# Kernel tuning notes

Measured on AMD Instinct MI355X. Metric: run time of the kernel, lower is better.

## Reference

```python
import jax, jax.numpy as jnp
import numpy as np

B = 2048      # number of binary mixtures
NPM = 30      # atoms per molecule
N = B * NPM   # total nodes per side
EPM = 120     # directed edges per molecule
IN_DIM = 74
H = 128
NC = 2


def setup_inputs() -> dict:
    key = jax.random.key(0)
    ks = jax.random.split(key, 24)
    rng = np.random.default_rng(0)
    off = np.repeat(np.arange(B, dtype=np.int64) * NPM, EPM)
    mk_idx = lambda: jnp.asarray((rng.integers(0, NPM, B * EPM) + off).astype(np.int32))

    def lin(k, fi, fo):
        return (jax.random.normal(k, (fi, fo), jnp.float32) / np.sqrt(fi)).astype(jnp.float32)

    inp = {
        'h1': jax.random.normal(ks[0], (N, IN_DIM), jnp.float32),
        'h2': jax.random.normal(ks[1], (N, IN_DIM), jnp.float32),
        'solv1_x': jax.random.uniform(ks[2], (B,), jnp.float32),
        'inter_hb': jax.random.uniform(ks[3], (B,), jnp.float32),
        'intra_hb1': jax.random.uniform(ks[4], (B,), jnp.float32),
        'intra_hb2': jax.random.uniform(ks[5], (B,), jnp.float32),
        'Wg1': lin(ks[6], IN_DIM, H), 'bg1': jnp.zeros((H,), jnp.float32),
        'Wg2': lin(ks[7], H, H), 'bg2': jnp.zeros((H,), jnp.float32),
        'Wp': lin(ks[8], H, H), 'bp': jnp.zeros((H,), jnp.float32),
        'We1': lin(ks[9], 1, 32), 'be1': jnp.zeros((32,), jnp.float32),
        'We2': lin(ks[10], 32, H * H), 'be2': jnp.zeros((H * H,), jnp.float32),
        'bnn': jnp.zeros((H,), jnp.float32),
        'Wih': lin(ks[11], H, 3 * H), 'bih': jnp.zeros((3 * H,), jnp.float32),
        'Whh': lin(ks[12], H, 3 * H), 'bhh': jnp.zeros((3 * H,), jnp.float32),
        'Wcl1': lin(ks[13], 2 * H, H), 'bcl1': jnp.zeros((H,), jnp.float32),
        'Wcl2': lin(ks[14], H, H), 'bcl2': jnp.zeros((H,), jnp.float32),
        'Wcl3': lin(ks[15], H, NC), 'bcl3': jnp.zeros((NC,), jnp.float32),
        'src1': mk_idx(), 'dst1': mk_idx(), 'src2': mk_idx(), 'dst2': mk_idx(),
    }
    return inp


def _graphconv(x, src, dst, W, b, n):
    # DGL GraphConv, norm='both': D_in^{-1/2} A D_out^{-1/2} X W + b
    ones = jnp.ones(src.shape[0], x.dtype)
    d_out = jnp.maximum(jax.ops.segment_sum(ones, src, num_segments=n), 1.0)
    d_in = jnp.maximum(jax.ops.segment_sum(ones, dst, num_segments=n), 1.0)
    m = (x * jax.lax.rsqrt(d_out)[:, None])[src]
    agg = jax.ops.segment_sum(m, dst, num_segments=n)
    return (agg * jax.lax.rsqrt(d_in)[:, None]) @ W + b


def _gru_step(x, h, Wih, bih, Whh, bhh):
    gi = x @ Wih + bih
    gh = h @ Whh + bhh
    ir, iz, ih = jnp.split(gi, 3, axis=-1)
    hr, hz, hn = jnp.split(gh, 3, axis=-1)
    r = jax.nn.sigmoid(ir + hr)
    z = jax.nn.sigmoid(iz + hz)
    n = jnp.tanh(ih + r * hn)
    return (1.0 - z) * n + z * h


def _forward(h1, h2, solv1_x, inter_hb, intra_hb1, intra_hb2,
             Wg1, bg1, Wg2, bg2, Wp, bp, We1, be1, We2, be2, bnn,
             Wih, bih, Whh, bhh, Wcl1, bcl1, Wcl2, bcl2, Wcl3, bcl3,
             src1, dst1, src2, dst2):
    # shared GraphConv layers on both molecule graphs
    t1 = jax.nn.relu(_graphconv(h1, src1, dst1, Wg1, bg1, N))
    t1 = jax.nn.relu(_graphconv(t1, src1, dst1, Wg2, bg2, N))
    t2 = jax.nn.relu(_graphconv(h2, src2, dst2, Wg1, bg1, N))
    t2 = jax.nn.relu(_graphconv(t2, src2, dst2, Wg2, bg2, N))
    # dgl.mean_nodes: per-molecule mean (uniform NPM nodes per molecule)
    hg1 = t1.reshape(B, NPM, H).mean(axis=1) * solv1_x[:, None]
    hg2 = t2.reshape(B, NPM, H).mean(axis=1) * (1.0 - solv1_x)[:, None]
    x = jnp.concatenate([hg1, hg2], axis=0)  # (2B, H)

    # empty_solvsys: inter edges i<->i+B (both dirs) then self-loops
    ar = jnp.arange(B, dtype=jnp.int32)
    ss = jnp.concatenate([ar, ar + B, ar, ar + B])
    sd = jnp.concatenate([ar + B, ar, ar, ar + B])
    ef = jnp.concatenate([inter_hb, inter_hb, intra_hb1, intra_hb2])[:, None]  # (4B,1)

    # MPNNconv: project, NNConv(sum) + GRU, 1 message-passing step
    x = jax.nn.relu(x @ Wp + bp)
    hstate = x
    for _ in range(1):
        w = (jax.nn.relu(ef @ We1 + be1) @ We2 + be2).reshape(-1, H, H)  # (4B,H,H)
        msg = jnp.einsum('ed,edf->ef', x[ss], w)
        agg = jax.ops.segment_sum(msg, sd, num_segments=2 * B) + bnn
        x = _gru_step(jax.nn.relu(agg), hstate, Wih, bih, Whh, bhh)
        hstate = x

    hg = jnp.concatenate([x[:B], x[B:]], axis=1)  # (B, 2H)
    o = jax.nn.relu(hg @ Wcl1 + bcl1)
    o = jax.nn.relu(o @ Wcl2 + bcl2)
    return o @ Wcl3 + bcl3


def reference(h1, h2, solv1_x, inter_hb, intra_hb1, intra_hb2,
              Wg1, bg1, Wg2, bg2, Wp, bp, We1, be1, We2, be2, bnn,
              Wih, bih, Whh, bhh, Wcl1, bcl1, Wcl2, bcl2, Wcl3, bcl3,
              src1, dst1, src2, dst2):
    return _forward(h1, h2, solv1_x, inter_hb, intra_hb1, intra_hb2,
                    Wg1, bg1, Wg2, bg2, Wp, bp, We1, be1, We2, be2, bnn,
                    Wih, bih, Whh, bhh, Wcl1, bcl1, Wcl2, bcl2, Wcl3, bcl3,
                    src1, dst1, src2, dst2)
```

## Files before the change

### kernel.cpp

```cpp
#include <hip/hip_runtime.h>
#include <hip/hip_bf16.h>
#include <math.h>

#define B2    2048
#define NPM   30
#define EPM   120

typedef __attribute__((ext_vector_type(8))) short short8;
typedef __attribute__((ext_vector_type(4))) float f32x4;

__device__ __forceinline__ ushort f2bf(float x) {
  unsigned u = __float_as_uint(x);
  return (ushort)((u + 0x7FFFu + ((u >> 16) & 1u)) >> 16);
}
__device__ __forceinline__ float bf2f(ushort h) {
  return __uint_as_float(((unsigned)h) << 16);
}

__device__ __forceinline__ int swz128(int r, int kb) { return r * 128 + (kb ^ ((r & 7) << 4)); }
__device__ __forceinline__ int swz256(int r, int kb) { return r * 256 + (kb ^ ((r & 15) << 4)); }

struct PrepDescs {
  const float* W[8];
  ushort* hi[8];
  ushort* lo[8];
  int Kreal[8], Kpad[8], N[8];
  int blk0[9];
};

__global__ __launch_bounds__(256) void prep_all_kernel(PrepDescs d)
{
  int b = blockIdx.x;
  int di = 0;
  #pragma unroll
  for (int j = 1; j < 8; ++j) if (b >= d.blk0[j]) di = j;
  int idx = (b - d.blk0[di]) * 256 + threadIdx.x;
  int Kp8 = d.Kpad[di] >> 3;
  int tot = d.N[di] * Kp8;
  if (idx >= tot) return;
  int n = idx / Kp8;
  int k8 = (idx - n * Kp8) << 3;
  const float* W = d.W[di];
  ushort* hi = d.hi[di];
  ushort* lo = d.lo[di];
  int Kreal = d.Kreal[di], Kpad = d.Kpad[di], N = d.N[di];
  #pragma unroll
  for (int j = 0; j < 8; ++j) {
    int k = k8 + j;
    float x = (k < Kreal) ? W[(long)k * N + n] : 0.f;
    ushort h = f2bf(x);
    hi[(long)n * Kpad + k] = h;
    lo[(long)n * Kpad + k] = f2bf(x - bf2f(h));
  }
}

__global__ __launch_bounds__(256) void prep_we2_kernel(
    const float* __restrict__ We2, ushort* __restrict__ hi, ushort* __restrict__ lo)
{
  int idx = blockIdx.x * 256 + threadIdx.x;
  int k = idx >> 11;
  int rem = idx & 2047;
  int n = rem >> 4;
  int d8 = (rem & 15) << 3;
  #pragma unroll
  for (int j = 0; j < 8; ++j) {
    int d = d8 + j;
    float x = We2[k * 16384 + d * 128 + n];
    ushort h = f2bf(x);
    hi[k * 16384 + n * 128 + d] = h;
    lo[k * 16384 + n * 128 + d] = f2bf(x - bf2f(h));
  }
}

__global__ __launch_bounds__(256, 2) void grufuse_kernel(
    const float* __restrict__ aggA, const float* __restrict__ aggB,
    const float* __restrict__ zb, const float* __restrict__ bnn,
    const float* __restrict__ xp,
    const ushort* __restrict__ Wihh, const ushort* __restrict__ Wihl,
    const float* __restrict__ bih,
    const ushort* __restrict__ Whhh, const ushort* __restrict__ Whhl,
    const float* __restrict__ bhh,
    float* __restrict__ xnew)
{
  __shared__ __align__(16) char A1h[16384], A1l[16384];
  __shared__ __align__(16) char A2h[16384], A2l[16384];
  __shared__ __align__(16) char Bh[8192], Bl[8192];
  const int tid = threadIdx.x;
  const int w = tid >> 6, l = tid & 63;
  const int rt = blockIdx.x >> 1;
  const int half = blockIdx.x & 1;
  const long rowBase = (long)rt * 64;
  const int ar = w * 16 + (l & 15);
  const int crow = w * 16 + ((l >> 4) << 2);

  #pragma unroll
  for (int q = 0; q < 8; ++q) {
    int t = tid + 256 * q;
    int r = t >> 5, k4 = (t & 31) << 2;
    long gr = rowBase + r;
    long i = (gr < B2) ? gr : (gr - B2);
    float4 za = *(const float4*)&zb[i * 128 + k4];
    float4 zc = *(const float4*)&zb[(i + B2) * 128 + k4];
    float4 bn = *(const float4*)&bnn[k4];
    const float* ap = (gr < B2) ? &aggA[i * 128 + k4] : &aggB[i * 128 + k4];
    float4 ag = *(const float4*)ap;
    float4 xv;
    xv.x = fmaxf(ag.x + za.x + zc.x + bn.x, 0.f);
    xv.y = fmaxf(ag.y + za.y + zc.y + bn.y, 0.f);
    xv.z = fmaxf(ag.z + za.z + zc.z + bn.z, 0.f);
    xv.w = fmaxf(ag.w + za.w + zc.w + bn.w, 0.f);
    ushort4 h4, l4;
    h4.x = f2bf(xv.x); l4.x = f2bf(xv.x - bf2f(h4.x));
    h4.y = f2bf(xv.y); l4.y = f2bf(xv.y - bf2f(h4.y));
    h4.z = f2bf(xv.z); l4.z = f2bf(xv.z - bf2f(h4.z));
    h4.w = f2bf(xv.w); l4.w = f2bf(xv.w - bf2f(h4.w));
    *(ushort4*)(A1h + swz256(r, k4 * 2)) = h4;
    *(ushort4*)(A1l + swz256(r, k4 * 2)) = l4;
    float4 pv = *(const float4*)&xp[gr * 128 + k4];
    h4.x = f2bf(pv.x); l4.x = f2bf(pv.x - bf2f(h4.x));
    h4.y = f2bf(pv.y); l4.y = f2bf(pv.y - bf2f(h4.y));
    h4.z = f2bf(pv.z); l4.z = f2bf(pv.z - bf2f(h4.z));
    h4.w = f2bf(pv.w); l4.w = f2bf(pv.w - bf2f(h4.w));
    *(ushort4*)(A2h + swz256(r, k4 * 2)) = h4;
    *(ushort4*)(A2l + swz256(r, k4 * 2)) = l4;
  }
  __syncthreads();

  f32x4 rg[4], zg[4];
  #pragma unroll
  for (int fc = 0; fc < 4; ++fc) { rg[fc] = (f32x4){0,0,0,0}; zg[fc] = (f32x4){0,0,0,0}; }

  for (int gate = 0; gate < 3; ++gate) {
    f32x4 gi[4], gh[4];
    #pragma unroll
    for (int fc = 0; fc < 4; ++fc) { gi[fc] = (f32x4){0,0,0,0}; gh[fc] = (f32x4){0,0,0,0}; }
    for (int src = 0; src < 2; ++src) {
      const ushort* Wh = src ? Whhh : Wihh;
      const ushort* Wl = src ? Whhl : Wihl;
      const char* Ah = src ? A2h : A1h;
      const char* Al = src ? A2l : A1l;
      f32x4* acc = src ? gh : gi;
      for (int k0 = 0; k0 < 128; k0 += 64) {
        __syncthreads();
        #pragma unroll
        for (int q = 0; q < 2; ++q) {
          int lin = tid + 256 * q;
          int n = lin >> 3, k8 = (lin & 7) << 3;
          long wrow = (long)(gate * 128 + half * 64 + n);
          *(uint4*)(Bh + swz128(n, k8 * 2)) = *(const uint4*)&Wh[wrow * 128 + k0 + k8];
          *(uint4*)(Bl + swz128(n, k8 * 2)) = *(const uint4*)&Wl[wrow * 128 + k0 + k8];
        }
        __syncthreads();
        #pragma unroll
        for (int ks = 0; ks < 2; ++ks) {
          const int ko = ks * 32 + (l >> 4) * 8;
          short8 ah  = *(const short8*)(Ah + swz256(ar, (k0 + ko) * 2));
          short8 al8 = *(const short8*)(Al + swz256(ar, (k0 + ko) * 2));
          #pragma unroll
          for (int fc = 0; fc < 4; ++fc) {
            const int c = fc * 16 + (l & 15);
            short8 bh  = *(const short8*)(Bh + swz128(c, ko * 2));
            short8 bl8 = *(const short8*)(Bl + swz128(c, ko * 2));
            acc[fc] = __builtin_amdgcn_mfma_f32_16x16x32_bf16(al8, bh, acc[fc], 0, 0, 0);
            acc[fc] = __builtin_amdgcn_mfma_f32_16x16x32_bf16(ah, bl8, acc[fc], 0, 0, 0);
            acc[fc] = __builtin_amdgcn_mfma_f32_16x16x32_bf16(ah, bh, acc[fc], 0, 0, 0);
          }
        }
      }
    }
    #pragma unroll
    for (int fc = 0; fc < 4; ++fc) {
      int cg = half * 64 + fc * 16 + (l & 15);
      float bi = bih[gate * 128 + cg], bh2 = bhh[gate * 128 + cg];
      #pragma unroll
      for (int i = 0; i < 4; ++i) {
        float a = gi[fc][i] + bi;
        float b = gh[fc][i] + bh2;
        if (gate == 0) {
          rg[fc][i] = 1.f / (1.f + expf(-(a + b)));
        } else if (gate == 1) {
          zg[fc][i] = 1.f / (1.f + expf(-(a + b)));
        } else {
          float ng = tanhf(a + rg[fc][i] * b);
          long row = rowBase + crow + i;
          float h = xp[row * 128 + cg];
          xnew[row * 128 + cg] = (1.f - zg[fc][i]) * ng + zg[fc][i] * h;
        }
      }
    }
  }
}

__global__ __launch_bounds__(256) void xpzb_kernel(
    const float* __restrict__ xcat,
    const ushort* __restrict__ Wph, const ushort* __restrict__ Wpl,
    const float* __restrict__ bp,
    const ushort* __restrict__ be2h, const ushort* __restrict__ be2l,
    float* __restrict__ xp, float* __restrict__ zb)
{
  __shared__ __align__(16) char AhB[16384], AlB[16384];
  __shared__ __align__(16) char BhB[16384], BlB[16384];
  const int tid = threadIdx.x;
  const int w = tid >> 6, l = tid & 63;
  const long rowBase = (long)blockIdx.x * 64;
  const int ar = w * 16 + (l & 15);
  const int crow = w * 16 + ((l >> 4) << 2);

  #pragma unroll
  for (int q = 0; q < 8; ++q) {
    int t = tid + 256 * q;
    int r = t >> 5, k4 = (t & 31) << 2;
    float4 v = *(const float4*)&xcat[(rowBase + r) * 128 + k4];
    ushort4 h4, l4;
    h4.x = f2bf(v.x); l4.x = f2bf(v.x - bf2f(h4.x));
    h4.y = f2bf(v.y); l4.y = f2bf(v.y - bf2f(h4.y));
    h4.z = f2bf(v.z); l4.z = f2bf(v.z - bf2f(h4.z));
    h4.w = f2bf(v.w); l4.w = f2bf(v.w - bf2f(h4.w));
    *(ushort4*)(AhB + swz256(r, k4 * 2)) = h4;
    *(ushort4*)(AlB + swz256(r, k4 * 2)) = l4;
  }
  __syncthreads();

  f32x4 acc[8];
  #pragma unroll
  for (int fc = 0; fc < 8; ++fc) acc[fc] = (f32x4){0.f, 0.f, 0.f, 0.f};
  for (int k0 = 0; k0 < 128; k0 += 64) {
    #pragma unroll
    for (int q = 0; q < 4; ++q) {
      int lin = tid + 256 * q;
      int n = lin >> 3, k8 = (lin & 7) << 3;
      *(uint4*)(BhB + swz128(n, k8 * 2)) = *(const uint4*)&Wph[n * 128 + k0 + k8];
      *(uint4*)(BlB + swz128(n, k8 * 2)) = *(const uint4*)&Wpl[n * 128 + k0 + k8];
    }
    __syncthreads();
    #pragma unroll
    for (int ks = 0; ks < 2; ++ks) {
      const int ko = ks * 32 + (l >> 4) * 8;
      short8 ah  = *(const short8*)(AhB + swz256(ar, (k0 + ko) * 2));
      short8 al8 = *(const short8*)(AlB + swz256(ar, (k0 + ko) * 2));
      #pragma unroll
      for (int fc = 0; fc < 8; ++fc) {
        const int c = fc * 16 + (l & 15);
        short8 bh  = *(const short8*)(BhB + swz128(c, ko * 2));
        short8 bl8 = *(const short8*)(BlB + swz128(c, ko * 2));
        acc[fc] = __builtin_amdgcn_mfma_f32_16x16x32_bf16(al8, bh, acc[fc], 0, 0, 0);
        acc[fc] = __builtin_amdgcn_mfma_f32_16x16x32_bf16(ah, bl8, acc[fc], 0, 0, 0);
        acc[fc] = __builtin_amdgcn_mfma_f32_16x16x32_bf16(ah, bh, acc[fc], 0, 0, 0);
      }
    }
    __syncthreads();
  }

  #pragma unroll
  for (int fc = 0; fc < 8; ++fc) {
    int col = fc * 16 + (l & 15);
    float bv = bp[col];
    #pragma unroll
    for (int i = 0; i < 4; ++i) {
      int lr = crow + i;
      float v = fmaxf(acc[fc][i] + bv, 0.f);
      xp[(rowBase + lr) * 128 + col] = v;
      ushort h = f2bf(v);
      *(ushort*)(AhB + swz256(lr, col * 2)) = h;
      *(ushort*)(AlB + swz256(lr, col * 2)) = f2bf(v - bf2f(h));
    }
  }

  #pragma unroll
  for (int fc = 0; fc < 8; ++fc) acc[fc] = (f32x4){0.f, 0.f, 0.f, 0.f};
  for (int k0 = 0; k0 < 128; k0 += 64) {
    __syncthreads();
    #pragma unroll
    for (int q = 0; q < 4; ++q) {
      int lin = tid + 256 * q;
      int n = lin >> 3, k8 = (lin & 7) << 3;
      *(uint4*)(BhB + swz128(n, k8 * 2)) = *(const uint4*)&be2h[n * 128 + k0 + k8];
      *(uint4*)(BlB + swz128(n, k8 * 2)) = *(const uint4*)&be2l[n * 128 + k0 + k8];
    }
    __syncthreads();
    #pragma unroll
    for (int ks = 0; ks < 2; ++ks) {
      const int ko = ks * 32 + (l >> 4) * 8;
      short8 ah  = *(const short8*)(AhB + swz256(ar, (k0 + ko) * 2));
      short8 al8 = *(const short8*)(AlB + swz256(ar, (k0 + ko) * 2));
      #pragma unroll
      for (int fc = 0; fc < 8; ++fc) {
        const int c = fc * 16 + (l & 15);
        short8 bh  = *(const short8*)(BhB + swz128(c, ko * 2));
        short8 bl8 = *(const short8*)(BlB + swz128(c, ko * 2));
        acc[fc] = __builtin_amdgcn_mfma_f32_16x16x32_bf16(al8, bh, acc[fc], 0, 0, 0);
        acc[fc] = __builtin_amdgcn_mfma_f32_16x16x32_bf16(ah, bl8, acc[fc], 0, 0, 0);
        acc[fc] = __builtin_amdgcn_mfma_f32_16x16x32_bf16(ah, bh, acc[fc], 0, 0, 0);
      }
    }
  }
  #pragma unroll
  for (int fc = 0; fc < 8; ++fc) {
    int col = fc * 16 + (l & 15);
    #pragma unroll
    for (int i = 0; i < 4; ++i) {
      int lr = crow + i;
      zb[(rowBase + lr) * 128 + col] = acc[fc][i];
    }
  }
}

__global__ __launch_bounds__(256) void cls_kernel(
    const float* __restrict__ xnew,
    const ushort* __restrict__ W1h, const ushort* __restrict__ W1l,
    const float* __restrict__ b1,
    const ushort* __restrict__ W2h, const ushort* __restrict__ W2l,
    const float* __restrict__ b2,
    const float* __restrict__ Wcl3, const float* __restrict__ bcl3,
    float* __restrict__ out)
{
  __shared__ __align__(16) char O1h[16384], O1l[16384];
  __shared__ __align__(16) char AhB[8192], AlB[8192];
  __shared__ __align__(16) char BhB[16384], BlB[16384];
  const int tid = threadIdx.x;
  const int w = tid >> 6, l = tid & 63;
  const long rowBase = (long)blockIdx.x * 64;
  const int ar = w * 16 + (l & 15);
  const int crow = w * 16 + ((l >> 4) << 2);

  f32x4 acc[8];
  #pragma unroll
  for (int fc = 0; fc < 8; ++fc) acc[fc] = (f32x4){0.f, 0.f, 0.f, 0.f};
  for (int k0 = 0; k0 < 256; k0 += 64) {
    const float* Ab = (k0 < 128) ? xnew : (xnew + (long)B2 * 128);
    const int kc = k0 & 127;
    #pragma unroll
    for (int q = 0; q < 4; ++q) {
      int lin = tid + 256 * q;
      int r = lin >> 4, k4 = (lin & 15) << 2;
      float4 v = *(const float4*)&Ab[(rowBase + r) * 128 + kc + k4];
      ushort4 h4, l4;
      h4.x = f2bf(v.x); l4.x = f2bf(v.x - bf2f(h4.x));
      h4.y = f2bf(v.y); l4.y = f2bf(v.y - bf2f(h4.y));
      h4.z = f2bf(v.z); l4.z = f2bf(v.z - bf2f(h4.z));
      h4.w = f2bf(v.w); l4.w = f2bf(v.w - bf2f(h4.w));
      *(ushort4*)(AhB + swz128(r, k4 * 2)) = h4;
      *(ushort4*)(AlB + swz128(r, k4 * 2)) = l4;
    }
    #pragma unroll
    for (int q = 0; q < 4; ++q) {
      int lin = tid + 256 * q;
      int n = lin >> 3, k8 = (lin & 7) << 3;
      *(uint4*)(BhB + swz128(n, k8 * 2)) = *(const uint4*)&W1h[(long)n * 256 + k0 + k8];
      *(uint4*)(BlB + swz128(n, k8 * 2)) = *(const uint4*)&W1l[(long)n * 256 + k0 + k8];
    }
    __syncthreads();
    #pragma unroll
    for (int ks = 0; ks < 2; ++ks) {
      const int ko = ks * 32 + (l >> 4) * 8;
      short8 ah  = *(const short8*)(AhB + swz128(ar, ko * 2));
      short8 al8 = *(const short8*)(AlB + swz128(ar, ko * 2));
      #pragma unroll
      for (int fc = 0; fc < 8; ++fc) {
        const int c = fc * 16 + (l & 15);
        short8 bh  = *(const short8*)(BhB + swz128(c, ko * 2));
        short8 bl8 = *(const short8*)(BlB + swz128(c, ko * 2));
        acc[fc] = __builtin_amdgcn_mfma_f32_16x16x32_bf16(al8, bh, acc[fc], 0, 0, 0);
        acc[fc] = __builtin_amdgcn_mfma_f32_16x16x32_bf16(ah, bl8, acc[fc], 0, 0, 0);
        acc[fc] = __builtin_amdgcn_mfma_f32_16x16x32_bf16(ah, bh, acc[fc], 0, 0, 0);
      }
    }
    __syncthreads();
  }
  #pragma unroll
  for (int fc = 0; fc < 8; ++fc) {
    int col = fc * 16 + (l & 15);
    float bv = b1[col];
    #pragma unroll
    for (int i = 0; i < 4; ++i) {
      int lr = crow + i;
      float v = fmaxf(acc[fc][i] + bv, 0.f);
      ushort h = f2bf(v);
      *(ushort*)(O1h + swz256(lr, col * 2)) = h;
      *(ushort*)(O1l + swz256(lr, col * 2)) = f2bf(v - bf2f(h));
    }
  }

  #pragma unroll
  for (int fc = 0; fc < 8; ++fc) acc[fc] = (f32x4){0.f, 0.f, 0.f, 0.f};
  for (int k0 = 0; k0 < 128; k0 += 64) {
    __syncthreads();
    #pragma unroll
    for (int q = 0; q < 4; ++q) {
      int lin = tid + 256 * q;
      int n = lin >> 3, k8 = (lin & 7) << 3;
      *(uint4*)(BhB + swz128(n, k8 * 2)) = *(const uint4*)&W2h[n * 128 + k0 + k8];
      *(uint4*)(BlB + swz128(n, k8 * 2)) = *(const uint4*)&W2l[n * 128 + k0 + k8];
    }
    __syncthreads();
    #pragma unroll
    for (int ks = 0; ks < 2; ++ks) {
      const int ko = ks * 32 + (l >> 4) * 8;
      short8 ah  = *(const short8*)(O1h + swz256(ar, (k0 + ko) * 2));
      short8 al8 = *(const short8*)(O1l + swz256(ar, (k0 + ko) * 2));
      #pragma unroll
      for (int fc = 0; fc < 8; ++fc) {
        const int c = fc * 16 + (l & 15);
        short8 bh  = *(const short8*)(BhB + swz128(c, ko * 2));
        short8 bl8 = *(const short8*)(BlB + swz128(c, ko * 2));
        acc[fc] = __builtin_amdgcn_mfma_f32_16x16x32_bf16(al8, bh, acc[fc], 0, 0, 0);
        acc[fc] = __builtin_amdgcn_mfma_f32_16x16x32_bf16(ah, bl8, acc[fc], 0, 0, 0);
        acc[fc] = __builtin_amdgcn_mfma_f32_16x16x32_bf16(ah, bh, acc[fc], 0, 0, 0);
      }
    }
  }

  float p0[4] = {0.f, 0.f, 0.f, 0.f}, p1[4] = {0.f, 0.f, 0.f, 0.f};
  #pragma unroll
  for (int fc = 0; fc < 8; ++fc) {
    int col = fc * 16 + (l & 15);
    float bv = b2[col];
    float w0 = Wcl3[col * 2], w1 = Wcl3[col * 2 + 1];
    #pragma unroll
    for (int i = 0; i < 4; ++i) {
      float v = fmaxf(acc[fc][i] + bv, 0.f);
      p0[i] = fmaf(v, w0, p0[i]);
      p1[i] = fmaf(v, w1, p1[i]);
    }
  }
  #pragma unroll
  for (int i = 0; i < 4; ++i) {
    #pragma unroll
    for (int m = 1; m < 16; m <<= 1) {
      p0[i] += __shfl_xor(p0[i], m);
      p1[i] += __shfl_xor(p1[i], m);
    }
    if ((l & 15) == 0) {
      long row = rowBase + crow + i;
      out[row * 2 + 0] = p0[i] + bcl3[0];
      out[row * 2 + 1] = p1[i] + bcl3[1];
    }
  }
}

__global__ __launch_bounds__(256, 1) void zfold_mfma_kernel(
    const float* __restrict__ xp,
    const ushort* __restrict__ We2h, const ushort* __restrict__ We2l,
    const float* __restrict__ interhb, const float* __restrict__ ia1,
    const float* __restrict__ ia2, const float* __restrict__ We1,
    const float* __restrict__ be1,
    float* __restrict__ aggA, float* __restrict__ aggB)
{
  __shared__ __align__(16) ushort Ah[2][64 * 72], Al[2][64 * 72];
  __shared__ __align__(16) ushort Bh[128 * 72], Bl[128 * 72];
  __shared__ float accAs[32 * 128], accBs[32 * 128];
  __shared__ float ehs[3][32][8];
  const int tid = threadIdx.x;
  const int w = tid >> 6, l = tid & 63;
  const int rg = blockIdx.x >> 2, kq = blockIdx.x & 3;
  const int i0 = rg * 32;

  for (int t = tid; t < 2048; t += 256) {
    int r = t >> 5, k4 = (t & 31) << 2;
    int gr = (r < 32) ? (i0 + r) : (B2 + i0 + r - 32);
    float4 v = *(const float4*)&xp[(long)gr * 128 + k4];
    int ch = k4 >> 6, ko = k4 & 63;
    ushort4 h4, l4;
    h4.x = f2bf(v.x); l4.x = f2bf(v.x - bf2f(h4.x));
    h4.y = f2bf(v.y); l4.y = f2bf(v.y - bf2f(h4.y));
    h4.z = f2bf(v.z); l4.z = f2bf(v.z - bf2f(h4.z));
    h4.w = f2bf(v.w); l4.w = f2bf(v.w - bf2f(h4.w));
    *(ushort4*)&Ah[ch][r * 72 + ko] = h4;
    *(ushort4*)&Al[ch][r * 72 + ko] = l4;
  }
  for (int t = tid; t < 768; t += 256) {
    int grp = t >> 8, rem = t & 255;
    int mm = rem >> 3, kk = rem & 7;
    int k = kq * 8 + kk;
    float u = (grp == 0) ? interhb[i0 + mm] : (grp == 1) ? ia1[i0 + mm] : ia2[i0 + mm];
    ehs[grp][mm][kk] = fmaxf(fmaf(u, We1[k], be1[k]), 0.f);
  }
  for (int t = tid; t < 4096; t += 256) { accAs[t] = 0.f; accBs[t] = 0.f; }

  float foldA[8][4] = {{0.f}}, foldB[8][4] = {{0.f}};
  const int ar = w * 16 + (l & 15);

  for (int kk = 0; kk < 8; ++kk) {
    const int k = kq * 8 + kk;
    f32x4 acc[8];
    #pragma unroll
    for (int fc = 0; fc < 8; ++fc) acc[fc] = (f32x4){0.f, 0.f, 0.f, 0.f};
    for (int ch = 0; ch < 2; ++ch) {
      __syncthreads();
      #pragma unroll
      for (int q = 0; q < 4; ++q) {
        int lin = tid + 256 * q;
        int n = lin >> 3, k8 = (lin & 7) << 3;
        *(uint4*)&Bh[n * 72 + k8] = *(const uint4*)&We2h[k * 16384 + n * 128 + ch * 64 + k8];
        *(uint4*)&Bl[n * 72 + k8] = *(const uint4*)&We2l[k * 16384 + n * 128 + ch * 64 + k8];
      }
      __syncthreads();
      #pragma unroll
      for (int ks = 0; ks < 2; ++ks) {
        const int ko = ks * 32 + (l >> 4) * 8;
        short8 ah  = *(const short8*)&Ah[ch][ar * 72 + ko];
        short8 al8 = *(const short8*)&Al[ch][ar * 72 + ko];
        #pragma unroll
        for (int fc = 0; fc < 8; ++fc) {
          const int c = fc * 16 + (l & 15);
          short8 bh  = *(const short8*)&Bh[c * 72 + ko];
          short8 bl8 = *(const short8*)&Bl[c * 72 + ko];
          acc[fc] = __builtin_amdgcn_mfma_f32_16x16x32_bf16(al8, bh, acc[fc], 0, 0, 0);
          acc[fc] = __builtin_amdgcn_mfma_f32_16x16x32_bf16(ah, bl8, acc[fc], 0, 0, 0);
          acc[fc] = __builtin_amdgcn_mfma_f32_16x16x32_bf16(ah, bh, acc[fc], 0, 0, 0);
        }
      }
    }
    #pragma unroll
    for (int i = 0; i < 4; ++i) {
      int lr = w * 16 + ((l >> 4) << 2) + i;
      int m = lr & 31, up = lr >> 5;
      float eA = up ? ehs[0][m][kk] : ehs[1][m][kk];
      float eB = up ? ehs[2][m][kk] : ehs[0][m][kk];
      #pragma unroll
      for (int fc = 0; fc < 8; ++fc) {
        foldA[fc][i] = fmaf(eA, acc[fc][i], foldA[fc][i]);
        foldB[fc][i] = fmaf(eB, acc[fc][i], foldB[fc][i]);
      }
    }
  }
  #pragma unroll
  for (int i = 0; i < 4; ++i) {
    int lr = w * 16 + ((l >> 4) << 2) + i;
    int m = lr & 31;
    #pragma unroll
    for (int fc = 0; fc < 8; ++fc) {
      int c = fc * 16 + (l & 15);
      atomicAdd(&accAs[m * 128 + c], foldA[fc][i]);
      atomicAdd(&accBs[m * 128 + c], foldB[fc][i]);
    }
  }
  __syncthreads();
  for (int t = tid; t < 4096; t += 256) {
    int mm = t >> 7, c = t & 127;
    atomicAdd(&aggA[(long)(i0 + mm) * 128 + c], accAs[t]);
    atomicAdd(&aggB[(long)(i0 + mm) * 128 + c], accBs[t]);
  }
}

__global__ __launch_bounds__(256) void adj_kernel(
    const int* __restrict__ src1, const int* __restrict__ dst1,
    const int* __restrict__ src2, const int* __restrict__ dst2,
    float* __restrict__ Abuf)
{
  __shared__ float cnt[4][30 * 33];
  __shared__ float rsOa[4][32], rsIa[4][32];
  const int tid = threadIdx.x, wid = tid >> 6, lane = tid & 63;
  const int gm = blockIdx.x * 4 + wid;
  const int g = gm >> 11, m = gm & 2047;
  const int* src = g ? src2 : src1;
  const int* dst = g ? dst2 : dst1;

  for (int i = lane; i < 30 * 33; i += 64) cnt[wid][i] = 0.f;
  __syncthreads();
  for (int e = lane; e < EPM; e += 64) {
    int s = src[m * EPM + e] - m * NPM;
    int d = dst[m * EPM + e] - m * NPM;
    atomicAdd(&cnt[wid][d * 33 + s], 1.0f);
  }
  __syncthreads();
  if (lane < NPM) {
    float sum = 0.f;
    for (int s = 0; s < NPM; ++s) sum += cnt[wid][lane * 33 + s];
    rsIa[wid][lane] = rsqrtf(fmaxf(sum, 1.f));
  } else if (lane >= 32 && lane < 32 + NPM) {
    int s = lane - 32; float sum = 0.f;
    for (int d = 0; d < NPM; ++d) sum += cnt[wid][d * 33 + s];
    rsOa[wid][s] = rsqrtf(fmaxf(sum, 1.f));
  }
  __syncthreads();
  const long base = (long)gm * 960;
  for (int i = lane; i < 960; i += 64) {
    int d = i >> 5, s = i & 31;
    float v = (d < NPM && s < NPM)
            ? cnt[wid][d * 33 + s] * rsIa[wid][d] * rsOa[wid][s] : 0.f;
    Abuf[base + i] = v;
  }
}

__global__ __launch_bounds__(512, 4) void gconv_kernel(
    const float* __restrict__ h1, const float* __restrict__ h2,
    const float* __restrict__ Abuf, const float* __restrict__ bg1,
    const ushort* __restrict__ W1h, const ushort* __restrict__ W1l,
    const ushort* __restrict__ W2h, const ushort* __restrict__ W2l,
    const float* __restrict__ bias2, const float* __restrict__ s1x,
    float* __restrict__ xcat)
{
  __shared__ __align__(16) char pool[66560];
  char* AhB = pool;
  char* AlB = pool + 16384;
  char* BhB = pool + 32768;
  char* BlB = pool + 49152;
  char* A2h = pool;
  char* A2l = pool + 8192;
  char* Byh = pool + 32768;
  char* Byl = pool + 49152;
  float* cs = (float*)(pool + 65536);

  const int tid = threadIdx.x;
  const int p = blockIdx.x;
  const int g = p >> 10;
  const int mloc = (p & 1023) * 2;
  const float* hsrc = g ? h2 : h1;
  if (tid < 256) cs[tid] = 0.f;

  const int w8 = tid >> 6, l = tid & 63;
  const int rw = w8 & 3;
  const int ch2 = w8 >> 2;
  const int ar = rw * 16 + (l & 15);
  const int crow = rw * 16 + ((l >> 4) << 2);

  #pragma unroll
  for (int q = 0; q < 4; ++q) {
    int lin = tid + 512 * q;
    int r = lin >> 5, k4 = (lin & 31) << 2;
    float4 v = make_float4(0.f, 0.f, 0.f, 0.f);
    if (r < 60) {
      const float* Ar = &hsrc[(long)(mloc * 30 + r) * 74];
      if (k4 + 4 <= 74) {
        float2 a = *(const float2*)&Ar[k4];
        float2 b = *(const float2*)&Ar[k4 + 2];
        v = make_float4(a.x, a.y, b.x, b.y);
      } else if (k4 + 2 <= 74) {
        float2 a = *(const float2*)&Ar[k4];
        v.x = a.x; v.y = a.y;
      }
    }
    ushort4 h4, l4;
    h4.x = f2bf(v.x); l4.x = f2bf(v.x - bf2f(h4.x));
    h4.y = f2bf(v.y); l4.y = f2bf(v.y - bf2f(h4.y));
    h4.z = f2bf(v.z); l4.z = f2bf(v.z - bf2f(h4.z));
    h4.w = f2bf(v.w); l4.w = f2bf(v.w - bf2f(h4.w));
    *(ushort4*)(AhB + swz256(r, k4 * 2)) = h4;
    *(ushort4*)(AlB + swz256(r, k4 * 2)) = l4;
  }
  __syncthreads();

  f32x4 acc[4];
  #pragma unroll
  for (int fc = 0; fc < 4; ++fc) acc[fc] = (f32x4){0.f, 0.f, 0.f, 0.f};
  for (int k0 = 0; k0 < 128; k0 += 64) {
    #pragma unroll
    for (int q = 0; q < 2; ++q) {
      int lin = tid + 512 * q;
      int n = lin >> 3, k8 = (lin & 7) << 3;
      *(uint4*)(BhB + swz128(n, k8 * 2)) = *(const uint4*)&W1h[n * 128 + k0 + k8];
      *(uint4*)(BlB + swz128(n, k8 * 2)) = *(const uint4*)&W1l[n * 128 + k0 + k8];
    }
    __syncthreads();
    #pragma unroll
    for (int ks = 0; ks < 2; ++ks) {
      const int ko = ks * 32 + (l >> 4) * 8;
      short8 ah  = *(const short8*)(AhB + swz256(ar, (k0 + ko) * 2));
      short8 al8 = *(const short8*)(AlB + swz256(ar, (k0 + ko) * 2));
      #pragma unroll
      for (int fc = 0; fc < 4; ++fc) {
        const int c = ch2 * 64 + fc * 16 + (l & 15);
        short8 bh  = *(const short8*)(BhB + swz128(c, ko * 2));
        short8 bl8 = *(const short8*)(BlB + swz128(c, ko * 2));
        acc[fc] = __builtin_amdgcn_mfma_f32_16x16x32_bf16(al8, bh, acc[fc], 0, 0, 0);
        acc[fc] = __builtin_amdgcn_mfma_f32_16x16x32_bf16(ah, bl8, acc[fc], 0, 0, 0);
        acc[fc] = __builtin_amdgcn_mfma_f32_16x16x32_bf16(ah, bh, acc[fc], 0, 0, 0);
      }
    }
    __syncthreads();
  }

  {
    const long ab0 = (long)(g * 2048 + mloc) * 960;
    for (int t = tid; t < 4096; t += 512) {
      int row = t >> 6, k = t & 63;
      float v = 0.f;
      if (row < 30) { if (k < 30) v = Abuf[ab0 + row * 32 + k]; }
      else if (row < 60) { if (k >= 30 && k < 60) v = Abuf[ab0 + 960 + (row - 30) * 32 + (k - 30)]; }
      ushort h = f2bf(v);
      *(ushort*)(A2h + swz128(row, k * 2)) = h;
      *(ushort*)(A2l + swz128(row, k * 2)) = f2bf(v - bf2f(h));
    }
  }
  #pragma unroll
  for (int fc = 0; fc < 4; ++fc) {
    int n = ch2 * 64 + fc * 16 + (l & 15);
    ushort4 h4, l4;
    h4.x = f2bf(acc[fc][0]); l4.x = f2bf(acc[fc][0] - bf2f(h4.x));
    h4.y = f2bf(acc[fc][1]); l4.y = f2bf(acc[fc][1] - bf2f(h4.y));
    h4.z = f2bf(acc[fc][2]); l4.z = f2bf(acc[fc][2] - bf2f(h4.z));
    h4.w = f2bf(acc[fc][3]); l4.w = f2bf(acc[fc][3] - bf2f(h4.w));
    *(ushort4*)(Byh + swz128(n, crow * 2)) = h4;
    *(ushort4*)(Byl + swz128(n, crow * 2)) = l4;
  }
  __syncthreads();

  f32x4 acc2[4];
  #pragma unroll
  for (int fc = 0; fc < 4; ++fc) acc2[fc] = (f32x4){0.f, 0.f, 0.f, 0.f};
  #pragma unroll
  for (int ks = 0; ks < 2; ++ks) {
    const int ko = ks * 32 + (l >> 4) * 8;
    short8 ah  = *(const short8*)(A2h + swz128(ar, ko * 2));
    short8 al8 = *(const short8*)(A2l + swz128(ar, ko * 2));
    #pragma unroll
    for (int fc = 0; fc < 4; ++fc) {
      const int c = ch2 * 64 + fc * 16 + (l & 15);
      short8 bh  = *(const short8*)(Byh + swz128(c, ko * 2));
      short8 bl8 = *(const short8*)(Byl + swz128(c, ko * 2));
      acc2[fc] = __builtin_amdgcn_mfma_f32_16x16x32_bf16(al8, bh, acc2[fc], 0, 0, 0);
      acc2[fc] = __builtin_amdgcn_mfma_f32_16x16x32_bf16(ah, bl8, acc2[fc], 0, 0, 0);
      acc2[fc] = __builtin_amdgcn_mfma_f32_16x16x32_bf16(ah, bh, acc2[fc], 0, 0, 0);
    }
  }
  __syncthreads();

  #pragma unroll
  for (int fc = 0; fc < 4; ++fc) {
    int n = ch2 * 64 + fc * 16 + (l & 15);
    float bv = bg1[n];
    float t0 = fmaxf(acc2[fc][0] + bv, 0.f);
    float t1v = fmaxf(acc2[fc][1] + bv, 0.f);
    float t2v = fmaxf(acc2[fc][2] + bv, 0.f);
    float t3 = fmaxf(acc2[fc][3] + bv, 0.f);
    ushort4 h4, l4;
    h4.x = f2bf(t0); l4.x = f2bf(t0 - bf2f(h4.x));
    h4.y = f2bf(t1v); l4.y = f2bf(t1v - bf2f(h4.y));
    h4.z = f2bf(t2v); l4.z = f2bf(t2v - bf2f(h4.z));
    h4.w = f2bf(t3); l4.w = f2bf(t3 - bf2f(h4.w));
    *(ushort4*)(Byh + swz128(n, crow * 2)) = h4;
    *(ushort4*)(Byl + swz128(n, crow * 2)) = l4;
  }
  __syncthreads();

  #pragma unroll
  for (int fc = 0; fc < 4; ++fc) acc2[fc] = (f32x4){0.f, 0.f, 0.f, 0.f};
  #pragma unroll
  for (int ks = 0; ks < 2; ++ks) {
    const int ko = ks * 32 + (l >> 4) * 8;
    short8 ah  = *(const short8*)(A2h + swz128(ar, ko * 2));
    short8 al8 = *(const short8*)(A2l + swz128(ar, ko * 2));
    #pragma unroll
    for (int fc = 0; fc < 4; ++fc) {
      const int c = ch2 * 64 + fc * 16 + (l & 15);
      short8 bh  = *(const short8*)(Byh + swz128(c, ko * 2));
      short8 bl8 = *(const short8*)(Byl + swz128(c, ko * 2));
      acc2[fc] = __builtin_amdgcn_mfma_f32_16x16x32_bf16(al8, bh, acc2[fc], 0, 0, 0);
      acc2[fc] = __builtin_amdgcn_mfma_f32_16x16x32_bf16(ah, bl8, acc2[fc], 0, 0, 0);
      acc2[fc] = __builtin_amdgcn_mfma_f32_16x16x32_bf16(ah, bh, acc2[fc], 0, 0, 0);
    }
  }
  __syncthreads();

  #pragma unroll
  for (int fc = 0; fc < 4; ++fc) {
    int n = ch2 * 64 + fc * 16 + (l & 15);
    #pragma unroll
    for (int i = 0; i < 4; ++i) {
      int r = crow + i;
      ushort h = f2bf(acc2[fc][i]);
      *(ushort*)(AhB + swz256(r, n * 2)) = h;
      *(ushort*)(AlB + swz256(r, n * 2)) = f2bf(acc2[fc][i] - bf2f(h));
    }
  }

  #pragma unroll
  for (int fc = 0; fc < 4; ++fc) acc[fc] = (f32x4){0.f, 0.f, 0.f, 0.f};
  for (int k0 = 0; k0 < 128; k0 += 64) {
    __syncthreads();
    #pragma unroll
    for (int q = 0; q < 2; ++q) {
      int lin = tid + 512 * q;
      int n = lin >> 3, k8 = (lin & 7) << 3;
      *(uint4*)(BhB + swz128(n, k8 * 2)) = *(const uint4*)&W2h[n * 128 + k0 + k8];
      *(uint4*)(BlB + swz128(n, k8 * 2)) = *(const uint4*)&W2l[n * 128 + k0 + k8];
    }
    __syncthreads();
    #pragma unroll
    for (int ks = 0; ks < 2; ++ks) {
      const int ko = ks * 32 + (l >> 4) * 8;
      short8 ah  = *(const short8*)(AhB + swz256(ar, (k0 + ko) * 2));
      short8 al8 = *(const short8*)(AlB + swz256(ar, (k0 + ko) * 2));
      #pragma unroll
      for (int fc = 0; fc < 4; ++fc) {
        const int c = ch2 * 64 + fc * 16 + (l & 15);
        short8 bh  = *(const short8*)(BhB + swz128(c, ko * 2));
        short8 bl8 = *(const short8*)(BlB + swz128(c, ko * 2));
        acc[fc] = __builtin_amdgcn_mfma_f32_16x16x32_bf16(al8, bh, acc[fc], 0, 0, 0);
        acc[fc] = __builtin_amdgcn_mfma_f32_16x16x32_bf16(ah, bl8, acc[fc], 0, 0, 0);
        acc[fc] = __builtin_amdgcn_mfma_f32_16x16x32_bf16(ah, bh, acc[fc], 0, 0, 0);
      }
    }
  }
  __syncthreads();

  #pragma unroll
  for (int fc = 0; fc < 4; ++fc) {
    int col = ch2 * 64 + fc * 16 + (l & 15);
    float bv = bias2[col];
    float s0 = 0.f, s1 = 0.f;
    #pragma unroll
    for (int i = 0; i < 4; ++i) {
      int lr = crow + i;
      if (lr < 60) {
        float v = fmaxf(acc[fc][i] + bv, 0.f);
        if (lr < NPM) s0 += v; else s1 += v;
      }
    }
    s0 += __shfl_down(s0, 32); s0 += __shfl_down(s0, 16);
    s1 += __shfl_down(s1, 32); s1 += __shfl_down(s1, 16);
    if ((l >> 4) == 0) {
      atomicAdd(&cs[col], s0);
      atomicAdd(&cs[128 + col], s1);
    }
  }
  __syncthreads();
  if (tid < 256) {
    int moll = tid >> 7, c = tid & 127;
    int gm = p * 2 + moll;
    int gg = gm >> 11, mm = gm & 2047;
    float sf = gg ? (1.f - s1x[mm]) : s1x[mm];
    xcat[(long)gm * 128 + c] = cs[moll * 128 + c] * (1.f / 30.f) * sf;
  }
}

extern "C" void kernel_launch(void* const* d_in, const int* in_sizes, int n_in,
                              void* d_out, int out_size, void* d_ws, size_t ws_size,
                              hipStream_t stream)
{
  const float* h1   = (const float*)d_in[0];
  const float* h2   = (const float*)d_in[1];
  const float* s1x  = (const float*)d_in[2];
  const float* ihb  = (const float*)d_in[3];
  const float* ia1  = (const float*)d_in[4];
  const float* ia2  = (const float*)d_in[5];
  const float* Wg1  = (const float*)d_in[6];
  const float* bg1  = (const float*)d_in[7];
  const float* Wg2  = (const float*)d_in[8];
  const float* bg2  = (const float*)d_in[9];
  const float* Wp   = (const float*)d_in[10];
  const float* bp   = (const float*)d_in[11];
  const float* We1  = (const float*)d_in[12];
  const float* be1  = (const float*)d_in[13];
  const float* We2  = (const float*)d_in[14];
  const float* be2  = (const float*)d_in[15];
  const float* bnn  = (const float*)d_in[16];
  const float* Wih  = (const float*)d_in[17];
  const float* bih  = (const float*)d_in[18];
  const float* Whh  = (const float*)d_in[19];
  const float* bhh  = (const float*)d_in[20];
  const float* Wcl1 = (const float*)d_in[21];
  const float* bcl1 = (const float*)d_in[22];
  const float* Wcl2 = (const float*)d_in[23];
  const float* bcl2 = (const float*)d_in[24];
  const float* Wcl3 = (const float*)d_in[25];
  const float* bcl3 = (const float*)d_in[26];
  const int*   src1 = (const int*)d_in[27];
  const int*   dst1 = (const int*)d_in[28];
  const int*   src2 = (const int*)d_in[29];
  const int*   dst2 = (const int*)d_in[30];
  float* out = (float*)d_out;
  float* ws  = (float*)d_ws;

  float* Abuf = ws;
  float* dwn  = ws + 35389440;

  float* xcat = dwn;
  float* xp   = dwn + 524288;
  float* zb   = dwn + 1048576;
  float* aggA = dwn + 1572864;
  float* aggB = dwn + 1835008;
  float* xnew = dwn + 2097152;

  ushort* wt     = (ushort*)(dwn + 6815744);
  ushort* WpTh   = wt;               ushort* WpTl   = wt + 16384;
  ushort* be2Th  = wt + 32768;       ushort* be2Tl  = wt + 49152;
  ushort* WihTh  = wt + 65536;       ushort* WihTl  = wt + 114688;
  ushort* WhhTh  = wt + 163840;      ushort* WhhTl  = wt + 212992;
  ushort* Wcl1Th = wt + 262144;      ushort* Wcl1Tl = wt + 294912;
  ushort* Wcl2Th = wt + 327680;      ushort* Wcl2Tl = wt + 344064;
  ushort* Wg1Th  = wt + 360448;      ushort* Wg1Tl  = wt + 376832;
  ushort* Wg2Th  = wt + 393216;      ushort* Wg2Tl  = wt + 409600;
  ushort* We2h   = wt + 425984;      ushort* We2l   = wt + 950272;

  PrepDescs pd;
  const float* Ws_[8]  = {Wp, be2, Wih, Whh, Wcl1, Wcl2, Wg1, Wg2};
  ushort* his[8]       = {WpTh, be2Th, WihTh, WhhTh, Wcl1Th, Wcl2Th, Wg1Th, Wg2Th};
  ushort* los[8]       = {WpTl, be2Tl, WihTl, WhhTl, Wcl1Tl, Wcl2Tl, Wg1Tl, Wg2Tl};
  int kr[8]   = {128, 128, 128, 128, 256, 128, 74, 128};
  int kp[8]   = {128, 128, 128, 128, 256, 128, 128, 128};
  int nn[8]   = {128, 128, 384, 384, 128, 128, 128, 128};
  int acc_blk = 0;
  for (int i = 0; i < 8; ++i) {
    pd.W[i] = Ws_[i]; pd.hi[i] = his[i]; pd.lo[i] = los[i];
    pd.Kreal[i] = kr[i]; pd.Kpad[i] = kp[i]; pd.N[i] = nn[i];
    pd.blk0[i] = acc_blk;
    acc_blk += (nn[i] * (kp[i] >> 3) + 255) / 256;
  }
  pd.blk0[8] = acc_blk;
  prep_all_kernel<<<acc_blk, 256, 0, stream>>>(pd);
  prep_we2_kernel<<<256, 256, 0, stream>>>(We2, We2h, We2l);

  adj_kernel<<<1024, 256, 0, stream>>>(src1, dst1, src2, dst2, Abuf);
  gconv_kernel<<<2048, 512, 0, stream>>>(h1, h2, Abuf, bg1, Wg1Th, Wg1Tl,
                                         Wg2Th, Wg2Tl, bg2, s1x, xcat);

  xpzb_kernel<<<64, 256, 0, stream>>>(xcat, WpTh, WpTl, bp, be2Th, be2Tl, xp, zb);
  hipMemsetAsync(aggA, 0, 2 * 262144 * sizeof(float), stream);
  zfold_mfma_kernel<<<256, 256, 0, stream>>>(xp, We2h, We2l, ihb, ia1, ia2,
                                             We1, be1, aggA, aggB);
  grufuse_kernel<<<128, 256, 0, stream>>>(aggA, aggB, zb, bnn, xp,
                                          WihTh, WihTl, bih, WhhTh, WhhTl, bhh,
                                          xnew);
  cls_kernel<<<32, 256, 0, stream>>>(xnew, Wcl1Th, Wcl1Tl, bcl1,
                                     Wcl2Th, Wcl2Tl, bcl2, Wcl3, bcl3, out);
}
```

Baseline: 200.1 us.

## Split GRU fusion kernel into smaller tiles for more blocks

```diff
diff --git a/kernel.cpp b/kernel.cpp
--- a/kernel.cpp
+++ b/kernel.cpp
@@ -72,7 +72,7 @@
   }
 }
 
-__global__ __launch_bounds__(256, 2) void grufuse_kernel(
+__global__ __launch_bounds__(256, 4) void grufuse_kernel(
     const float* __restrict__ aggA, const float* __restrict__ aggB,
     const float* __restrict__ zb, const float* __restrict__ bnn,
     const float* __restrict__ xp,
@@ -82,19 +82,21 @@
     const float* __restrict__ bhh,
     float* __restrict__ xnew)
 {
-  __shared__ __align__(16) char A1h[16384], A1l[16384];
-  __shared__ __align__(16) char A2h[16384], A2l[16384];
-  __shared__ __align__(16) char Bh[8192], Bl[8192];
+  __shared__ __align__(16) char A1h[8192], A1l[8192];
+  __shared__ __align__(16) char A2h[8192], A2l[8192];
+  __shared__ __align__(16) char Bh[4096], Bl[4096];
   const int tid = threadIdx.x;
   const int w = tid >> 6, l = tid & 63;
-  const int rt = blockIdx.x >> 1;
-  const int half = blockIdx.x & 1;
-  const long rowBase = (long)rt * 64;
-  const int ar = w * 16 + (l & 15);
-  const int crow = w * 16 + ((l >> 4) << 2);
-
-  #pragma unroll
-  for (int q = 0; q < 8; ++q) {
+  const int rt = blockIdx.x >> 2;
+  const int qt = blockIdx.x & 3;
+  const long rowBase = (long)rt * 32;
+  const int rw = w & 1;
+  const int cs = w >> 1;
+  const int ar = rw * 16 + (l & 15);
+  const int crow = rw * 16 + ((l >> 4) << 2);
+
+  #pragma unroll
+  for (int q = 0; q < 4; ++q) {
     int t = tid + 256 * q;
     int r = t >> 5, k4 = (t & 31) << 2;
     long gr = rowBase + r;
@@ -126,66 +128,55 @@
   }
   __syncthreads();
 
-  f32x4 rg[4], zg[4];
-  #pragma unroll
-  for (int fc = 0; fc < 4; ++fc) { rg[fc] = (f32x4){0,0,0,0}; zg[fc] = (f32x4){0,0,0,0}; }
+  f32x4 rg = (f32x4){0,0,0,0}, zg = (f32x4){0,0,0,0};
 
   for (int gate = 0; gate < 3; ++gate) {
-    f32x4 gi[4], gh[4];
-    #pragma unroll
-    for (int fc = 0; fc < 4; ++fc) { gi[fc] = (f32x4){0,0,0,0}; gh[fc] = (f32x4){0,0,0,0}; }
+    f32x4 gi = (f32x4){0,0,0,0}, gh = (f32x4){0,0,0,0};
     for (int src = 0; src < 2; ++src) {
       const ushort* Wh = src ? Whhh : Wihh;
       const ushort* Wl = src ? Whhl : Wihl;
       const char* Ah = src ? A2h : A1h;
       const char* Al = src ? A2l : A1l;
-      f32x4* acc = src ? gh : gi;
       for (int k0 = 0; k0 < 128; k0 += 64) {
         __syncthreads();
-        #pragma unroll
-        for (int q = 0; q < 2; ++q) {
-          int lin = tid + 256 * q;
-          int n = lin >> 3, k8 = (lin & 7) << 3;
-          long wrow = (long)(gate * 128 + half * 64 + n);
+        {
+          int n = tid >> 3, k8 = (tid & 7) << 3;
+          long wrow = (long)(gate * 128 + qt * 32 + n);
           *(uint4*)(Bh + swz128(n, k8 * 2)) = *(const uint4*)&Wh[wrow * 128 + k0 + k8];
           *(uint4*)(Bl + swz128(n, k8 * 2)) = *(const uint4*)&Wl[wrow * 128 + k0 + k8];
         }
         __syncthreads();
+        f32x4 a = (src == 0) ? gi : gh;
         #pragma unroll
         for (int ks = 0; ks < 2; ++ks) {
           const int ko = ks * 32 + (l >> 4) * 8;
           short8 ah  = *(const short8*)(Ah + swz256(ar, (k0 + ko) * 2));
           short8 al8 = *(const short8*)(Al + swz256(ar, (k0 + ko) * 2));
-          #pragma unroll
-          for (int fc = 0; fc < 4; ++fc) {
-            const int c = fc * 16 + (l & 15);
-            short8 bh  = *(const short8*)(Bh + swz128(c, ko * 2));
-            short8 bl8 = *(const short8*)(Bl + swz128(c, ko * 2));
-            acc[fc] = __builtin_amdgcn_mfma_f32_16x16x32_bf16(al8, bh, acc[fc], 0, 0, 0);
-            acc[fc] = __builtin_amdgcn_mfma_f32_16x16x32_bf16(ah, bl8, acc[fc], 0, 0, 0);
-            acc[fc] = __builtin_amdgcn_mfma_f32_16x16x32_bf16(ah, bh, acc[fc], 0, 0, 0);
-          }
+          const int c = cs * 16 + (l & 15);
+          short8 bh  = *(const short8*)(Bh + swz128(c, ko * 2));
+          short8 bl8 = *(const short8*)(Bl + swz128(c, ko * 2));
+          a = __builtin_amdgcn_mfma_f32_16x16x32_bf16(al8, bh, a, 0, 0, 0);
+          a = __builtin_amdgcn_mfma_f32_16x16x32_bf16(ah, bl8, a, 0, 0, 0);
+          a = __builtin_amdgcn_mfma_f32_16x16x32_bf16(ah, bh, a, 0, 0, 0);
         }
-      }
-    }
-    #pragma unroll
-    for (int fc = 0; fc < 4; ++fc) {
-      int cg = half * 64 + fc * 16 + (l & 15);
-      float bi = bih[gate * 128 + cg], bh2 = bhh[gate * 128 + cg];
-      #pragma unroll
-      for (int i = 0; i < 4; ++i) {
-        float a = gi[fc][i] + bi;
-        float b = gh[fc][i] + bh2;
-        if (gate == 0) {
-          rg[fc][i] = 1.f / (1.f + expf(-(a + b)));
-        } else if (gate == 1) {
-          zg[fc][i] = 1.f / (1.f + expf(-(a + b)));
-        } else {
-          float ng = tanhf(a + rg[fc][i] * b);
-          long row = rowBase + crow + i;
-          float h = xp[row * 128 + cg];
-          xnew[row * 128 + cg] = (1.f - zg[fc][i]) * ng + zg[fc][i] * h;
-        }
+        if (src == 0) gi = a; else gh = a;
+      }
+    }
+    int cg = qt * 32 + cs * 16 + (l & 15);
+    float bi = bih[gate * 128 + cg], bh2 = bhh[gate * 128 + cg];
+    #pragma unroll
+    for (int i = 0; i < 4; ++i) {
+      float a = gi[i] + bi;
+      float b = gh[i] + bh2;
+      if (gate == 0) {
+        rg[i] = 1.f / (1.f + expf(-(a + b)));
+      } else if (gate == 1) {
+        zg[i] = 1.f / (1.f + expf(-(a + b)));
+      } else {
+        float ng = tanhf(a + rg[i] * b);
+        long row = rowBase + crow + i;
+        float h = xp[row * 128 + cg];
+        xnew[row * 128 + cg] = (1.f - zg[i]) * ng + zg[i] * h;
       }
     }
   }
@@ -910,7 +901,7 @@
   hipMemsetAsync(aggA, 0, 2 * 262144 * sizeof(float), stream);
   zfold_mfma_kernel<<<256, 256, 0, stream>>>(xp, We2h, We2l, ihb, ia1, ia2,
                                              We1, be1, aggA, aggB);
-  grufuse_kernel<<<128, 256, 0, stream>>>(aggA, aggB, zb, bnn, xp,
+  grufuse_kernel<<<512, 256, 0, stream>>>(aggA, aggB, zb, bnn, xp,
                                           WihTh, WihTl, bih, WhhTh, WhhTl, bhh,
                                           xnew);
   cls_kernel<<<32, 256, 0, stream>>>(xnew, Wcl1Th, Wcl1Tl, bcl1,
```

Measured after the change: 181.6 us (median of 2 runs). 9.3% less time.
